# Kernel tuning notes

Measured on AMD Instinct MI355X. Metric: run time of the kernel, lower is better.

## Reference

```python
import jax, jax.numpy as jnp
import numpy as np

G = 128  # voxel grid extent per axis (positions are integer voxel coords in [0, G))
K = 3    # kernel size per axis -> 27 offsets


def setup_inputs() -> dict:
    key = jax.random.key(0)
    k1, k2, k3 = jax.random.split(key, 3)
    N, Cin, Cout = 500000, 32, 32
    features = jax.random.normal(k1, (N, Cin), dtype=jnp.float32)
    in_positions = jax.random.randint(k2, (N, 3), 0, G, dtype=jnp.int32)
    # learned conv weight: one [Cin, Cout] matrix per kernel offset (27 total)
    weight = jax.random.normal(k3, (K ** 3, Cin, Cout), dtype=jnp.float32) * 0.05
    return {"features": features, "in_positions": in_positions, "weight": weight}


def _hash(pos):
    # unique linear key for integer voxel coords in [0, G)^3
    return (pos[:, 0] * G + pos[:, 1]) * G + pos[:, 2]


def reference(features, in_positions, weight):
    # Submanifold sparse conv (kernel 3x3x3, odd -> offset 0, out_positions == in_positions,
    # voxel_size = 1.0, no bias, no normalize):
    # for each active voxel, gather active neighbors at each of the 27 kernel offsets,
    # transform with the per-offset weight matrix, and accumulate.
    N = features.shape[0]
    # dense hash table: voxel key -> row index in features, -1 if inactive
    table = jnp.full((G * G * G,), -1, dtype=jnp.int32)
    table = table.at[_hash(in_positions)].set(jnp.arange(N, dtype=jnp.int32))

    out = jnp.zeros((N, weight.shape[-1]), dtype=features.dtype)
    r = K // 2
    k = 0
    for dx in range(-r, r + 1):
        for dy in range(-r, r + 1):
            for dz in range(-r, r + 1):
                npos = in_positions + jnp.array([dx, dy, dz], dtype=jnp.int32)
                inside = jnp.all((npos >= 0) & (npos < G), axis=1)
                idx = table[jnp.where(inside, _hash(npos), 0)]
                valid = inside & (idx >= 0)
                # gather active neighbor features; zero where neighbor inactive
                gathered = jnp.where(valid[:, None], features[jnp.maximum(idx, 0)], 0.0)
                out = out + gathered @ weight[k]  # [N, Cout]
                k += 1
    return out
```

## Files before the change

kernel.cpp:

```cpp
#include <hip/hip_runtime.h>


#define GRID 128
#define CIN 32
#define COUT 32
#define NOFF 27
#define TILE 16

typedef __attribute__((ext_vector_type(8))) short bf16x8;
typedef __attribute__((ext_vector_type(4))) float f32x4;

__device__ inline unsigned short f2bf(float x) {
    union { float f; unsigned u; } v; v.f = x;
    unsigned r = v.u + 0x7fff + ((v.u >> 16) & 1);
    return (unsigned short)(r >> 16);
}

__global__ void scatter_kernel(const int* __restrict__ pos,
                               int* __restrict__ table, int N) {
    int i = blockIdx.x * blockDim.x + threadIdx.x;
    if (i >= N) return;
    int x = pos[3 * i], y = pos[3 * i + 1], z = pos[3 * i + 2];
    atomicMax(&table[(x * GRID + y) * GRID + z], i);
}

__global__ void convert_wt(const float* __restrict__ wt,
                           unsigned short* __restrict__ wtT) {
    int t = blockIdx.x * 256 + threadIdx.x;
    if (t >= NOFF * CIN * COUT) return;
    int k = t >> 10, r = t & 1023, ci = r >> 5, co = r & 31;
    wtT[k * 1024 + co * 32 + ci] = f2bf(wt[t]);
}

__global__ void convert_feats(const float* __restrict__ f,
                              unsigned* __restrict__ fb, int elems4) {
    int i = blockIdx.x * blockDim.x + threadIdx.x;
    if (i >= elems4) return;
    float4 v = *(const float4*)(f + 4 * (size_t)i);
    unsigned lo = (unsigned)f2bf(v.x) | ((unsigned)f2bf(v.y) << 16);
    unsigned hi = (unsigned)f2bf(v.z) | ((unsigned)f2bf(v.w) << 16);
    uint2 o; o.x = lo; o.y = hi;
    *(uint2*)(fb + 2 * (size_t)i) = o;
}

__global__ __launch_bounds__(256, 5)
void conv_kernel(const unsigned short* __restrict__ featsB,
                 const int* __restrict__ pos,
                 const unsigned short* __restrict__ wtT,
                 const int* __restrict__ table,
                 float* __restrict__ out, int N, int numTiles) {
    int gtid = blockIdx.x * 256 + threadIdx.x;
    int tile = gtid >> 6;
    if (tile >= numTiles) return;
    int lane = threadIdx.x & 63;
    int m = lane & 15, quad = lane >> 4;
    int base = tile * TILE;
    int g = base + m;
    bool gv = g < N;

    int x = 0, y = 0, z = 0;
    if (gv) { x = pos[3 * g]; y = pos[3 * g + 1]; z = pos[3 * g + 2]; }

    f32x4 acc0 = {0.f, 0.f, 0.f, 0.f};
    f32x4 acc1 = {0.f, 0.f, 0.f, 0.f};
    const unsigned short* wb = wtT + quad * 8;

#pragma unroll
    for (int k = 0; k < NOFF; ++k) {
        const int dx = k / 9 - 1, dy = (k / 3) % 3 - 1, dz = k % 3 - 1;
        int nx = x + dx, ny = y + dy, nz = z + dz;
        int id = -1;
        if (gv && (unsigned)nx < GRID && (unsigned)ny < GRID && (unsigned)nz < GRID)
            id = table[(nx * GRID + ny) * GRID + nz];

        bf16x8 a = {0, 0, 0, 0, 0, 0, 0, 0};
        if (id >= 0)
            a = *(const bf16x8*)(featsB + (size_t)id * CIN + quad * 8);

        bf16x8 b0 = *(const bf16x8*)(wb + k * 1024 + m * 32);
        bf16x8 b1 = *(const bf16x8*)(wb + k * 1024 + (m + 16) * 32);

        acc0 = __builtin_amdgcn_mfma_f32_16x16x32_bf16(a, b0, acc0, 0, 0, 0);
        acc1 = __builtin_amdgcn_mfma_f32_16x16x32_bf16(a, b1, acc1, 0, 0, 0);
    }

#pragma unroll
    for (int i = 0; i < 4; ++i) {
        int go = base + quad * 4 + i;
        if (go < N) {
            out[(size_t)go * COUT + m]      = acc0[i];
            out[(size_t)go * COUT + m + 16] = acc1[i];
        }
    }
}

extern "C" void kernel_launch(void* const* d_in, const int* in_sizes, int n_in,
                              void* d_out, int out_size, void* d_ws, size_t ws_size,
                              hipStream_t stream) {
    const float* feats = (const float*)d_in[0];
    const int*   pos   = (const int*)d_in[1];
    const float* wt    = (const float*)d_in[2];
    float* out = (float*)d_out;
    int N = in_sizes[0] / CIN;

    char* ws = (char*)d_ws;
    int* table = (int*)ws;
    size_t table_bytes = (size_t)GRID * GRID * GRID * sizeof(int);
    unsigned short* wtT = (unsigned short*)(ws + table_bytes);
    unsigned short* featsB = (unsigned short*)(ws + table_bytes + 65536);

    hipMemsetAsync(table, 0xFF, table_bytes, stream);

    int sb = 256;
    scatter_kernel<<<(N + sb - 1) / sb, sb, 0, stream>>>(pos, table, N);

    int wtElems = NOFF * CIN * COUT;
    convert_wt<<<(wtElems + 255) / 256, 256, 0, stream>>>(wt, wtT);

    int elems4 = N * CIN / 4;
    convert_feats<<<(elems4 + 255) / 256, 256, 0, stream>>>(
        feats, (unsigned*)featsB, elems4);

    int numTiles = (N + TILE - 1) / TILE;
    int waves = numTiles;
    int blocks = (waves + 3) / 4;
    conv_kernel<<<blocks, 256, 0, stream>>>(featsB, pos, wtT, table, out, N, numTiles);
}
```

Measured before the change: 317.1 us.

## Process 64 points per wave with shuffled lookups and fuse prep kernels

Each wave now handles 64 voxels instead of 16. Every lane does its own hash-table lookup, and the neighbour indices are distributed with wave shuffles, so the per-offset weight fragments are loaded once and reused across four MFMA sub-tiles. The table scatter, feature conversion and weight transpose are merged into a single prep launch to cut launch overhead. The cost is more accumulator registers (occupancy hint lowered from 5 to 4) and fewer waves overall, which gives less parallelism for hiding gather latency.

```diff
diff --git a/kernel.cpp b/kernel.cpp
--- a/kernel.cpp
+++ b/kernel.cpp
@@ -5,7 +5,7 @@
 #define CIN 32
 #define COUT 32
 #define NOFF 27
-#define TILE 16
+#define MT 64
 
 typedef __attribute__((ext_vector_type(8))) short bf16x8;
 typedef __attribute__((ext_vector_type(4))) float f32x4;
@@ -16,34 +16,32 @@
     return (unsigned short)(r >> 16);
 }
 
-__global__ void scatter_kernel(const int* __restrict__ pos,
-                               int* __restrict__ table, int N) {
-    int i = blockIdx.x * blockDim.x + threadIdx.x;
-    if (i >= N) return;
-    int x = pos[3 * i], y = pos[3 * i + 1], z = pos[3 * i + 2];
-    atomicMax(&table[(x * GRID + y) * GRID + z], i);
+__global__ void prep_kernel(const float* __restrict__ feats,
+                            const int* __restrict__ pos,
+                            const float* __restrict__ wt,
+                            int* __restrict__ table,
+                            unsigned* __restrict__ featsB,
+                            unsigned short* __restrict__ wtT,
+                            int N, int elems4) {
+    int i = blockIdx.x * 256 + threadIdx.x;
+    if (i < elems4) {
+        float4 v = *(const float4*)(feats + 4 * (size_t)i);
+        unsigned lo = (unsigned)f2bf(v.x) | ((unsigned)f2bf(v.y) << 16);
+        unsigned hi = (unsigned)f2bf(v.z) | ((unsigned)f2bf(v.w) << 16);
+        uint2 o; o.x = lo; o.y = hi;
+        *(uint2*)(featsB + 2 * (size_t)i) = o;
+    }
+    if (i < N) {
+        int x = pos[3 * i], y = pos[3 * i + 1], z = pos[3 * i + 2];
+        atomicMax(&table[(x * GRID + y) * GRID + z], i);
+    }
+    if (i < NOFF * CIN * COUT) {
+        int k = i >> 10, r = i & 1023, ci = r >> 5, co = r & 31;
+        wtT[k * 1024 + co * 32 + ci] = f2bf(wt[i]);
+    }
 }
 
-__global__ void convert_wt(const float* __restrict__ wt,
-                           unsigned short* __restrict__ wtT) {
-    int t = blockIdx.x * 256 + threadIdx.x;
-    if (t >= NOFF * CIN * COUT) return;
-    int k = t >> 10, r = t & 1023, ci = r >> 5, co = r & 31;
-    wtT[k * 1024 + co * 32 + ci] = f2bf(wt[t]);
-}
-
-__global__ void convert_feats(const float* __restrict__ f,
-                              unsigned* __restrict__ fb, int elems4) {
-    int i = blockIdx.x * blockDim.x + threadIdx.x;
-    if (i >= elems4) return;
-    float4 v = *(const float4*)(f + 4 * (size_t)i);
-    unsigned lo = (unsigned)f2bf(v.x) | ((unsigned)f2bf(v.y) << 16);
-    unsigned hi = (unsigned)f2bf(v.z) | ((unsigned)f2bf(v.w) << 16);
-    uint2 o; o.x = lo; o.y = hi;
-    *(uint2*)(fb + 2 * (size_t)i) = o;
-}
-
-__global__ __launch_bounds__(256, 5)
+__global__ __launch_bounds__(256, 4)
 void conv_kernel(const unsigned short* __restrict__ featsB,
                  const int* __restrict__ pos,
                  const unsigned short* __restrict__ wtT,
@@ -54,15 +52,20 @@
     if (tile >= numTiles) return;
     int lane = threadIdx.x & 63;
     int m = lane & 15, quad = lane >> 4;
-    int base = tile * TILE;
-    int g = base + m;
+    int base = tile * MT;
+    int g = base + lane;
     bool gv = g < N;
 
     int x = 0, y = 0, z = 0;
     if (gv) { x = pos[3 * g]; y = pos[3 * g + 1]; z = pos[3 * g + 2]; }
 
-    f32x4 acc0 = {0.f, 0.f, 0.f, 0.f};
-    f32x4 acc1 = {0.f, 0.f, 0.f, 0.f};
+    f32x4 acc[4][2];
+#pragma unroll
+    for (int f = 0; f < 4; ++f)
+#pragma unroll
+        for (int h = 0; h < 2; ++h)
+            acc[f][h] = (f32x4){0.f, 0.f, 0.f, 0.f};
+
     const unsigned short* wb = wtT + quad * 8;
 
 #pragma unroll
@@ -73,23 +76,29 @@
         if (gv && (unsigned)nx < GRID && (unsigned)ny < GRID && (unsigned)nz < GRID)
             id = table[(nx * GRID + ny) * GRID + nz];
 
-        bf16x8 a = {0, 0, 0, 0, 0, 0, 0, 0};
-        if (id >= 0)
-            a = *(const bf16x8*)(featsB + (size_t)id * CIN + quad * 8);
-
         bf16x8 b0 = *(const bf16x8*)(wb + k * 1024 + m * 32);
         bf16x8 b1 = *(const bf16x8*)(wb + k * 1024 + (m + 16) * 32);
 
-        acc0 = __builtin_amdgcn_mfma_f32_16x16x32_bf16(a, b0, acc0, 0, 0, 0);
-        acc1 = __builtin_amdgcn_mfma_f32_16x16x32_bf16(a, b1, acc1, 0, 0, 0);
+#pragma unroll
+        for (int f = 0; f < 4; ++f) {
+            int idf = __shfl(id, f * 16 + m, 64);
+            bf16x8 a = {0, 0, 0, 0, 0, 0, 0, 0};
+            if (idf >= 0)
+                a = *(const bf16x8*)(featsB + (size_t)idf * CIN + quad * 8);
+            acc[f][0] = __builtin_amdgcn_mfma_f32_16x16x32_bf16(a, b0, acc[f][0], 0, 0, 0);
+            acc[f][1] = __builtin_amdgcn_mfma_f32_16x16x32_bf16(a, b1, acc[f][1], 0, 0, 0);
+        }
     }
 
 #pragma unroll
-    for (int i = 0; i < 4; ++i) {
-        int go = base + quad * 4 + i;
-        if (go < N) {
-            out[(size_t)go * COUT + m]      = acc0[i];
-            out[(size_t)go * COUT + m + 16] = acc1[i];
+    for (int f = 0; f < 4; ++f) {
+#pragma unroll
+        for (int i = 0; i < 4; ++i) {
+            int p = base + f * 16 + quad * 4 + i;
+            if (p < N) {
+                out[(size_t)p * COUT + m]      = acc[f][0][i];
+                out[(size_t)p * COUT + m + 16] = acc[f][1][i];
+            }
         }
     }
 }
@@ -111,18 +120,11 @@
 
     hipMemsetAsync(table, 0xFF, table_bytes, stream);
 
-    int sb = 256;
-    scatter_kernel<<<(N + sb - 1) / sb, sb, 0, stream>>>(pos, table, N);
+    int elems4 = N * CIN / 4;
+    prep_kernel<<<(elems4 + 255) / 256, 256, 0, stream>>>(
+        feats, pos, wt, table, (unsigned*)featsB, wtT, N, elems4);
 
-    int wtElems = NOFF * CIN * COUT;
-    convert_wt<<<(wtElems + 255) / 256, 256, 0, stream>>>(wt, wtT);
-
-    int elems4 = N * CIN / 4;
-    convert_feats<<<(elems4 + 255) / 256, 256, 0, stream>>>(
-        feats, (unsigned*)featsB, elems4);
-
-    int numTiles = (N + TILE - 1) / TILE;
-    int waves = numTiles;
-    int blocks = (waves + 3) / 4;
+    int numTiles = (N + MT - 1) / MT;
+    int blocks = (numTiles + 3) / 4;
     conv_kernel<<<blocks, 256, 0, stream>>>(featsB, pos, wtT, table, out, N, numTiles);
 }
```

Result: no change. 322.6 us (+1.7%).
